# Performance work log

Hardware: AMD Instinct MI355X
Metric: run time of the kernel (lower is better)

The kernel has to match this reference:

```python
import jax, jax.numpy as jnp
import numpy as np

STRIDE = 2

def _conv_transpose3d(x, w_io, stride):
    # x: [N, I, D, H, W]; w_io: [I, O, k2, k3, k4] (torch conv_transpose layout)
    # conv_transpose == lhs-dilated conv with spatially-flipped, IO-swapped kernel
    rhs = jnp.flip(jnp.transpose(w_io, (1, 0, 2, 3, 4)), axis=(2, 3, 4))  # [O, I, k2, k3, k4]
    ks = w_io.shape[2:]
    pad = [(k - 1, k - 1) for k in ks]
    return jax.lax.conv_general_dilated(
        x, rhs, window_strides=(1, 1, 1), padding=pad,
        lhs_dilation=(stride, stride, stride),
        dimension_numbers=('NCDHW', 'OIDHW', 'NCDHW'))


def setup_inputs() -> dict:
    key = jax.random.key(0)
    k1, k2, k3 = jax.random.split(key, 3)
    B, Cin, Cout = 4, 64, 64
    K = (3, 3, 3, 3)
    L = (12, 12, 12, 12)
    init_norm = float(np.sqrt(1.0 / Cout / np.prod(K)))
    x = jax.random.normal(k1, (B, Cin, *L), dtype=jnp.float32)
    weight = init_norm * (2.0 * jax.random.normal(k2, (Cin, Cout, *K), dtype=jnp.float32) - 1.0)
    bias = init_norm * (2.0 * jax.random.normal(k3, (Cout,), dtype=jnp.float32) - 1.0)
    return {'x': x, 'weight': weight, 'bias': bias}


def reference(x, weight, bias):
    # 4D transposed convolution, stride=STRIDE, no padding/dilation, groups=1.
    B, I, L1, L2, L3, L4 = x.shape
    _, O, K1, K2, K3, K4 = weight.shape
    s = STRIDE
    o1 = (L1 - 1) * s + K1
    o2 = (L2 - 1) * s + K2
    o3 = (L3 - 1) * s + K3
    o4 = (L4 - 1) * s + K4
    # Fold first spatial dim into batch; do 3D conv_transpose over the remaining dims.
    xb = jnp.transpose(x, (0, 2, 1, 3, 4, 5)).reshape(B * L1, I, L2, L3, L4)
    out = jnp.zeros((B, O, o1, o2, o3, o4), dtype=x.dtype)
    for ik in range(K1):  # small fixed kernel loop
        y = _conv_transpose3d(xb, weight[:, :, ik], s)           # [B*L1, O, o2, o3, o4]
        y = jnp.transpose(y.reshape(B, L1, O, o2, o3, o4), (0, 2, 1, 3, 4, 5))
        out = out.at[:, :, ik:ik + L1 * s:s].add(y)              # strided scatter-add along dim 1
    out = out + bias[None, :, None, None, None, None]
    return out
```

## Files before the change

### kernel.cpp

```cpp
#include <hip/hip_runtime.h>


typedef short bf16x8 __attribute__((ext_vector_type(8)));
typedef float f32x4 __attribute__((ext_vector_type(4)));

__device__ __forceinline__ unsigned short f2bf(float f) {
    unsigned int u = __float_as_uint(f);
    u = (u + 0x7FFFu + ((u >> 16) & 1u)) >> 16;
    return (unsigned short)u;
}

__global__ __launch_bounds__(256) void wtrans_kernel(const float* __restrict__ w,
                                                     unsigned short* __restrict__ wt) {
    int tid = blockIdx.x * 256 + threadIdx.x;
    if (tid >= 81 * 64 * 64) return;
    int ci = tid & 63;
    int co = (tid >> 6) & 63;
    int kk = tid >> 12;
    wt[tid] = f2bf(w[(ci * 64 + co) * 81 + kk]);
}

__global__ __launch_bounds__(256) void xtrans_kernel(const float* __restrict__ x,
                                                     unsigned short* __restrict__ xb) {
    __shared__ unsigned short ls[144][72];
    int blk = blockIdx.x;
    int i2 = blk % 12; int t = blk / 12; int i1 = t % 12; int b = t / 12;
    int tid = threadIdx.x;
    int ci = tid >> 2, sub = tid & 3;
    const float* src = x + (size_t)b * 1327104 + (size_t)ci * 20736 + i1 * 1728 + i2 * 144 + sub * 36;
    #pragma unroll
    for (int q = 0; q < 9; ++q) {
        float4 v = *(const float4*)(src + q * 4);
        #pragma unroll
        for (int u = 0; u < 4; ++u) ls[sub * 36 + q * 4 + u][ci] = f2bf(((const float*)&v)[u]);
    }
    __syncthreads();
    unsigned short* dst = xb + (size_t)blk * 9216;
    for (int c = tid; c < 1152; c += 256) {
        int m = c >> 3, part = c & 7;
        *(bf16x8*)(dst + c * 8) = *(const bf16x8*)((const char*)ls + m * 144 + part * 16);
    }
}

#define XS_BYTES 25088
#define WS_BYTES 24576
#define SMEM_BYTES 49664

__global__ __launch_bounds__(512, 2) void convt_mfma_kernel(
        const unsigned short* __restrict__ xb,
        const unsigned short* __restrict__ wt,
        const float* __restrict__ bias,
        float* __restrict__ out) {

    __shared__ __align__(16) char smem[SMEM_BYTES];
    char* xsb = smem;
    char* wsb = smem + XS_BYTES;
    float (*stg)[625] = (float (*)[625])smem;

    int orig = blockIdx.x;
    int xcd = orig & 7, oj = orig >> 3;
    int wg = (xcd < 4 ? xcd * 313 : 1252 + (xcd - 4) * 312) + oj;
    int p2 = wg % 25; int tq = wg / 25;
    int p1 = tq % 25; int b = tq / 25;

    int i1v[2], k1v[2], n1 = 0;
    { int h = p1 >> 1, q = p1 & 1;
      for (int s = 0; s < 2 - q; ++s) { int i = h - s; if (0 <= i && i < 12) { i1v[n1] = i; k1v[n1] = 2 * s + q; ++n1; } } }
    int i2v[2], k2v[2], n2 = 0;
    { int h = p2 >> 1, q = p2 & 1;
      for (int s = 0; s < 2 - q; ++s) { int i = h - s; if (0 <= i && i < 12) { i2v[n2] = i; k2v[n2] = 2 * s + q; ++n2; } } }
    int ncomb = n1 * n2;

    int tid = threadIdx.x;
    int lane = tid & 63;
    int wave = __builtin_amdgcn_readfirstlane(tid >> 6);
    int n_lo = lane & 15, quad = lane >> 4;

    static const int NSLOT[8] = {4, 4, 5, 5, 5, 5, 6, 6};
    static const signed char SCLS[8][6] = {
        {0,0,2,2,0,0}, {0,0,2,2,0,0}, {0,0,3,3,3,0}, {0,0,3,3,3,0},
        {0,0,3,3,3,0}, {0,1,1,2,2,0}, {1,1,1,1,2,2}, {1,1,1,1,2,2}};
    static const signed char STILE[8][6] = {
        {0,1,0,1,0,0}, {2,3,2,3,0,0}, {4,5,0,1,2,0}, {6,7,3,4,5,0},
        {8,9,6,7,8,0}, {10,0,1,4,5,0}, {2,3,4,5,6,7}, {6,7,8,9,8,9}};

    int ns = NSLOT[wave];
    int use0 = 0, use1 = 0, use2 = 0, use3 = 0;
    int rbase[6]; unsigned vis = 0;
    #pragma unroll
    for (int j = 0; j < 6; ++j) {
        int c = SCLS[wave][j], t = STILE[wave][j];
        int r3 = c >> 1, r4 = c & 1;
        int n4 = 13 - r4, N = (13 - r3) * n4;
        int pos = t * 16 + n_lo;
        int cp = pos < N ? pos : N - 1;
        int pe3 = cp / n4, pe4 = cp - pe3 * n4;
        rbase[j] = (pe3 + 1) * 14 + (pe4 + 1);
        if (j < ns) {
            if (pos < N) vis |= 1u << j;
            use0 |= (c == 0); use1 |= (c == 1); use2 |= (c == 2); use3 |= (c == 3);
        }
    }

    for (int f = tid; f < XS_BYTES / 4; f += 512) ((int*)xsb)[f] = 0;

    f32x4 acc[6][4];
    #pragma unroll
    for (int mt = 0; mt < 4; ++mt) {
        #pragma unroll
        for (int rg = 0; rg < 4; ++rg) {
            float bv = bias[mt * 16 + quad * 4 + rg];
            #pragma unroll
            for (int j = 0; j < 6; ++j) acc[j][mt][rg] = bv;
        }
    }
    __syncthreads();

    for (int c = 0; c < ncomb; ++c) {
        if (c) __syncthreads();
        int c1 = c / n2, c2 = c - (c / n2) * n2;
        int i1 = i1v[c1], k1 = k1v[c1];
        int i2 = i2v[c2], k2 = k2v[c2];

        const unsigned short* xbs = xb + (size_t)((b * 12 + i1) * 12 + i2) * 9216;
        #pragma unroll
        for (int it = 0; it < 3; ++it) {
            int idx = it * 512 + tid;
            if (idx < 1152) {
                bf16x8 v = *(const bf16x8*)(xbs + idx * 8);
                int m = idx >> 3, part = idx & 7;
                int a3 = (m * 2731) >> 15, a4 = m - a3 * 12;
                int r = (a3 + 1) * 14 + a4 + 1;
                *(bf16x8*)(xsb + r * 128 + ((part ^ (r & 7)) << 4)) = v;
            }
        }

        int kb9 = (k1 * 3 + k2) * 9;
        for (int g = 0; g < 3; ++g) {
            if (g) __syncthreads();
            const unsigned short* wsrc = wt + (size_t)(kb9 + 3 * g) * 4096;
            #pragma unroll
            for (int it = 0; it < 3; ++it) {
                int idx = it * 512 + tid;
                bf16x8 v = *(const bf16x8*)(wsrc + idx * 8);
                int tap = idx >> 9, rch = idx & 511;
                int co = rch >> 3, part = rch & 7;
                *(bf16x8*)(wsb + tap * 8192 + co * 128 + ((part ^ (co & 7)) << 4)) = v;
            }
            __syncthreads();

            int p = g & 1, s3 = (g - p) >> 1;
            #pragma unroll
            for (int tap = 0; tap < 3; ++tap) {
                const int par = tap & 1;
                int any = par ? (p ? use3 : use1) : (p ? use2 : use0);
                if (!any) continue;
                int s4 = tap >> 1;
                const char* wst = wsb + tap * 8192;
                int need = 2 * p + par;
                #pragma unroll
                for (int kc = 0; kc < 2; ++kc) {
                    int pr = kc * 4 + quad;
                    int pwa = (pr ^ (n_lo & 7)) << 4;
                    bf16x8 a0  = *(const bf16x8*)(wst + n_lo * 128 + pwa);
                    bf16x8 a1  = *(const bf16x8*)(wst + n_lo * 128 + 2048 + pwa);
                    bf16x8 a2  = *(const bf16x8*)(wst + n_lo * 128 + 4096 + pwa);
                    bf16x8 a3v = *(const bf16x8*)(wst + n_lo * 128 + 6144 + pwa);
                    #pragma unroll
                    for (int j = 0; j < 6; ++j) {
                        if (j < ns && SCLS[wave][j] == need) {
                            int row = rbase[j] - s3 * 14 - s4;
                            bf16x8 bb = *(const bf16x8*)(xsb + row * 128 + ((pr ^ (row & 7)) << 4));
                            acc[j][0] = __builtin_amdgcn_mfma_f32_16x16x32_bf16(a0,  bb, acc[j][0], 0, 0, 0);
                            acc[j][1] = __builtin_amdgcn_mfma_f32_16x16x32_bf16(a1,  bb, acc[j][1], 0, 0, 0);
                            acc[j][2] = __builtin_amdgcn_mfma_f32_16x16x32_bf16(a2,  bb, acc[j][2], 0, 0, 0);
                            acc[j][3] = __builtin_amdgcn_mfma_f32_16x16x32_bf16(a3v, bb, acc[j][3], 0, 0, 0);
                        }
                    }
                }
            }
        }
    }

    __syncthreads();

    size_t obase = (size_t)b * 64 * 390625 + (size_t)(p1 * 25 + p2) * 625;
    #pragma unroll
    for (int ch = 0; ch < 4; ++ch) {
        #pragma unroll
        for (int j = 0; j < 6; ++j) {
            if ((vis >> j) & 1) {
                int cc = SCLS[wave][j];
                int r3 = cc >> 1, r4 = cc & 1;
                int rb = rbase[j] - 15;
                int pe3 = (rb * 2341) >> 15;
                int pe4 = rb - 14 * pe3;
                int p34 = (2 * pe3 + r3) * 25 + 2 * pe4 + r4;
                #pragma unroll
                for (int rg = 0; rg < 4; ++rg)
                    stg[quad * 4 + rg][p34] = acc[j][ch][rg];
            }
        }
        __syncthreads();
        for (int idx2 = tid; idx2 < 10000; idx2 += 512) {
            int co_l = idx2 / 625, e = idx2 - 625 * co_l;
            out[obase + (size_t)(ch * 16 + co_l) * 390625 + e] = stg[co_l][e];
        }
        __syncthreads();
    }
}

extern "C" void kernel_launch(void* const* d_in, const int* in_sizes, int n_in,
                              void* d_out, int out_size, void* d_ws, size_t ws_size,
                              hipStream_t stream) {
    const float* x    = (const float*)d_in[0];
    const float* w    = (const float*)d_in[1];
    const float* bias = (const float*)d_in[2];
    float* out = (float*)d_out;
    unsigned short* wt = (unsigned short*)d_ws;
    unsigned short* xbf = wt + 81 * 64 * 64;

    wtrans_kernel<<<(81 * 64 * 64 + 255) / 256, 256, 0, stream>>>(w, wt);
    xtrans_kernel<<<576, 256, 0, stream>>>(x, xbf);
    convt_mfma_kernel<<<2500, 512, 0, stream>>>(xbf, wt, bias, out);
}
```

Measured before the change: 580.9 us.

## Double-buffer weight groups with register prefetch and rebalance wave tile slots

```diff
diff --git a/kernel.cpp b/kernel.cpp
--- a/kernel.cpp
+++ b/kernel.cpp
@@ -11,13 +11,12 @@
 }
 
 __global__ __launch_bounds__(256) void wtrans_kernel(const float* __restrict__ w,
-                                                     unsigned short* __restrict__ wt) {
+                                                     unsigned short* __restrict__ wt2) {
     int tid = blockIdx.x * 256 + threadIdx.x;
     if (tid >= 81 * 64 * 64) return;
-    int ci = tid & 63;
-    int co = (tid >> 6) & 63;
-    int kk = tid >> 12;
-    wt[tid] = f2bf(w[(ci * 64 + co) * 81 + kk]);
+    int u = tid & 7, co = (tid >> 3) & 63, pr = (tid >> 9) & 7, kk = tid >> 12;
+    int ci = pr * 8 + u;
+    wt2[tid] = f2bf(w[(ci * 64 + co) * 81 + kk]);
 }
 
 __global__ __launch_bounds__(256) void xtrans_kernel(const float* __restrict__ x,
@@ -43,12 +42,12 @@
 }
 
 #define XS_BYTES 25088
-#define WS_BYTES 24576
-#define SMEM_BYTES 49664
+#define WS_HALF  24576
+#define SMEM_BYTES (XS_BYTES + 2 * WS_HALF)
 
 __global__ __launch_bounds__(512, 2) void convt_mfma_kernel(
         const unsigned short* __restrict__ xb,
-        const unsigned short* __restrict__ wt,
+        const unsigned short* __restrict__ wt2,
         const float* __restrict__ bias,
         float* __restrict__ out) {
 
@@ -76,123 +75,138 @@
     int wave = __builtin_amdgcn_readfirstlane(tid >> 6);
     int n_lo = lane & 15, quad = lane >> 4;
 
-    static const int NSLOT[8] = {4, 4, 5, 5, 5, 5, 6, 6};
-    static const signed char SCLS[8][6] = {
-        {0,0,2,2,0,0}, {0,0,2,2,0,0}, {0,0,3,3,3,0}, {0,0,3,3,3,0},
-        {0,0,3,3,3,0}, {0,1,1,2,2,0}, {1,1,1,1,2,2}, {1,1,1,1,2,2}};
-    static const signed char STILE[8][6] = {
-        {0,1,0,1,0,0}, {2,3,2,3,0,0}, {4,5,0,1,2,0}, {6,7,3,4,5,0},
-        {8,9,6,7,8,0}, {10,0,1,4,5,0}, {2,3,4,5,6,7}, {6,7,8,9,8,9}};
-
-    int ns = NSLOT[wave];
-    int use0 = 0, use1 = 0, use2 = 0, use3 = 0;
-    int rbase[6]; unsigned vis = 0;
-    #pragma unroll
-    for (int j = 0; j < 6; ++j) {
-        int c = SCLS[wave][j], t = STILE[wave][j];
-        int r3 = c >> 1, r4 = c & 1;
-        int n4 = 13 - r4, N = (13 - r3) * n4;
+    static const signed char SCLS5[8][5] = {
+        {0,0,1,2,3},{0,0,1,2,3},{0,0,1,2,3},
+        {0,1,1,2,2},{0,1,1,2,2},
+        {0,1,2,3,3},{0,1,2,3,3},{0,1,2,3,3}};
+    static const signed char STILE5[8][5] = {
+        {0,1,0,0,0},{2,3,1,1,1},{4,5,2,2,2},
+        {6,3,4,3,4},{7,5,6,5,6},
+        {8,7,7,3,4},{9,8,8,5,6},{10,9,9,7,8}};
+
+    int cmask = 0;
+    int rb128[5]; unsigned vis = 0;
+    #pragma unroll
+    for (int j = 0; j < 5; ++j) {
+        int cs = SCLS5[wave][j], t = STILE5[wave][j];
+        int r3 = cs >> 1, r4 = cs & 1;
+        int n4c = 13 - r4, Nc = (13 - r3) * n4c;
         int pos = t * 16 + n_lo;
-        int cp = pos < N ? pos : N - 1;
-        int pe3 = cp / n4, pe4 = cp - pe3 * n4;
-        rbase[j] = (pe3 + 1) * 14 + (pe4 + 1);
-        if (j < ns) {
-            if (pos < N) vis |= 1u << j;
-            use0 |= (c == 0); use1 |= (c == 1); use2 |= (c == 2); use3 |= (c == 3);
-        }
-    }
+        int cp = pos < Nc ? pos : Nc - 1;
+        int pe3 = cp / n4c, pe4 = cp - pe3 * n4c;
+        rb128[j] = ((pe3 + 1) * 14 + (pe4 + 1)) << 7;
+        if (pos < Nc) vis |= 1u << j;
+        cmask |= 1 << cs;
+    }
+
+    int xsw0, xsw1, xsw2;
+    {
+        #pragma unroll
+        for (int it = 0; it < 3; ++it) {
+            int idx = it * 512 + tid;
+            int m = idx >> 3, part = idx & 7;
+            int a3 = (m * 2731) >> 15, a4 = m - a3 * 12;
+            int r = (a3 + 1) * 14 + a4 + 1;
+            int v = r * 128 + ((part ^ (r & 7)) << 4);
+            if (it == 0) xsw0 = v; else if (it == 1) xsw1 = v; else xsw2 = v;
+        }
+    }
+    int wsw = tid * 16;
+    int abase = quad * 1024 + n_lo * 16;
 
     for (int f = tid; f < XS_BYTES / 4; f += 512) ((int*)xsb)[f] = 0;
 
-    f32x4 acc[6][4];
+    f32x4 acc[5][4];
     #pragma unroll
     for (int mt = 0; mt < 4; ++mt) {
         #pragma unroll
         for (int rg = 0; rg < 4; ++rg) {
             float bv = bias[mt * 16 + quad * 4 + rg];
             #pragma unroll
-            for (int j = 0; j < 6; ++j) acc[j][mt][rg] = bv;
+            for (int j = 0; j < 5; ++j) acc[j][mt][rg] = bv;
         }
     }
     __syncthreads();
 
+#define COMPUTE_GROUP(G, WB) do {                                              \
+    const int s3_ = (G) >> 1;                                                  \
+    _Pragma("unroll")                                                          \
+    for (int tap = 0; tap < 3; ++tap) {                                        \
+        int need = 2 * ((G) & 1) + (tap & 1), s4 = tap >> 1;                   \
+        if (!((cmask >> need) & 1)) continue;                                  \
+        const char* wt_ = (WB) + tap * 8192;                                   \
+        _Pragma("unroll")                                                      \
+        for (int kc = 0; kc < 2; ++kc) {                                       \
+            const char* ab = wt_ + kc * 4096 + abase;                          \
+            bf16x8 a0  = *(const bf16x8*)(ab);                                 \
+            bf16x8 a1  = *(const bf16x8*)(ab + 256);                           \
+            bf16x8 a2  = *(const bf16x8*)(ab + 512);                           \
+            bf16x8 a3v = *(const bf16x8*)(ab + 768);                           \
+            int prq = kc * 4 + quad;                                           \
+            _Pragma("unroll")                                                  \
+            for (int j = 0; j < 5; ++j) {                                      \
+                if (SCLS5[wave][j] == need) {                                  \
+                    int row128 = rb128[j] - ((s3_ * 14 + s4) << 7);            \
+                    int r7 = (row128 >> 7) & 7;                                \
+                    bf16x8 bb = *(const bf16x8*)(xsb + row128 + ((prq ^ r7) << 4)); \
+                    acc[j][0] = __builtin_amdgcn_mfma_f32_16x16x32_bf16(a0,  bb, acc[j][0], 0, 0, 0); \
+                    acc[j][1] = __builtin_amdgcn_mfma_f32_16x16x32_bf16(a1,  bb, acc[j][1], 0, 0, 0); \
+                    acc[j][2] = __builtin_amdgcn_mfma_f32_16x16x32_bf16(a2,  bb, acc[j][2], 0, 0, 0); \
+                    acc[j][3] = __builtin_amdgcn_mfma_f32_16x16x32_bf16(a3v, bb, acc[j][3], 0, 0, 0); \
+                }                                                              \
+            }                                                                  \
+        }                                                                      \
+    } } while (0)
+
     for (int c = 0; c < ncomb; ++c) {
-        if (c) __syncthreads();
         int c1 = c / n2, c2 = c - (c / n2) * n2;
         int i1 = i1v[c1], k1 = k1v[c1];
         int i2 = i2v[c2], k2 = k2v[c2];
-
-        const unsigned short* xbs = xb + (size_t)((b * 12 + i1) * 12 + i2) * 9216;
-        #pragma unroll
-        for (int it = 0; it < 3; ++it) {
-            int idx = it * 512 + tid;
-            if (idx < 1152) {
-                bf16x8 v = *(const bf16x8*)(xbs + idx * 8);
-                int m = idx >> 3, part = idx & 7;
-                int a3 = (m * 2731) >> 15, a4 = m - a3 * 12;
-                int r = (a3 + 1) * 14 + a4 + 1;
-                *(bf16x8*)(xsb + r * 128 + ((part ^ (r & 7)) << 4)) = v;
-            }
-        }
-
         int kb9 = (k1 * 3 + k2) * 9;
-        for (int g = 0; g < 3; ++g) {
-            if (g) __syncthreads();
-            const unsigned short* wsrc = wt + (size_t)(kb9 + 3 * g) * 4096;
-            #pragma unroll
-            for (int it = 0; it < 3; ++it) {
-                int idx = it * 512 + tid;
-                bf16x8 v = *(const bf16x8*)(wsrc + idx * 8);
-                int tap = idx >> 9, rch = idx & 511;
-                int co = rch >> 3, part = rch & 7;
-                *(bf16x8*)(wsb + tap * 8192 + co * 128 + ((part ^ (co & 7)) << 4)) = v;
-            }
-            __syncthreads();
-
-            int p = g & 1, s3 = (g - p) >> 1;
-            #pragma unroll
-            for (int tap = 0; tap < 3; ++tap) {
-                const int par = tap & 1;
-                int any = par ? (p ? use3 : use1) : (p ? use2 : use0);
-                if (!any) continue;
-                int s4 = tap >> 1;
-                const char* wst = wsb + tap * 8192;
-                int need = 2 * p + par;
-                #pragma unroll
-                for (int kc = 0; kc < 2; ++kc) {
-                    int pr = kc * 4 + quad;
-                    int pwa = (pr ^ (n_lo & 7)) << 4;
-                    bf16x8 a0  = *(const bf16x8*)(wst + n_lo * 128 + pwa);
-                    bf16x8 a1  = *(const bf16x8*)(wst + n_lo * 128 + 2048 + pwa);
-                    bf16x8 a2  = *(const bf16x8*)(wst + n_lo * 128 + 4096 + pwa);
-                    bf16x8 a3v = *(const bf16x8*)(wst + n_lo * 128 + 6144 + pwa);
-                    #pragma unroll
-                    for (int j = 0; j < 6; ++j) {
-                        if (j < ns && SCLS[wave][j] == need) {
-                            int row = rbase[j] - s3 * 14 - s4;
-                            bf16x8 bb = *(const bf16x8*)(xsb + row * 128 + ((pr ^ (row & 7)) << 4));
-                            acc[j][0] = __builtin_amdgcn_mfma_f32_16x16x32_bf16(a0,  bb, acc[j][0], 0, 0, 0);
-                            acc[j][1] = __builtin_amdgcn_mfma_f32_16x16x32_bf16(a1,  bb, acc[j][1], 0, 0, 0);
-                            acc[j][2] = __builtin_amdgcn_mfma_f32_16x16x32_bf16(a2,  bb, acc[j][2], 0, 0, 0);
-                            acc[j][3] = __builtin_amdgcn_mfma_f32_16x16x32_bf16(a3v, bb, acc[j][3], 0, 0, 0);
-                        }
-                    }
-                }
-            }
-        }
-    }
-
-    __syncthreads();
+        const bf16x8* wgsrc = (const bf16x8*)wt2 + (size_t)kb9 * 512;
+
+        bf16x8 wv0 = wgsrc[tid], wv1 = wgsrc[tid + 512], wv2 = wgsrc[tid + 1024];
+        const bf16x8* xbs = (const bf16x8*)(xb + (size_t)((b * 12 + i1) * 12 + i2) * 9216);
+        bf16x8 x0 = xbs[tid], x1 = xbs[tid + 512];
+        bf16x8 x2; if (tid < 128) x2 = xbs[tid + 1024];
+
+        char* wb0 = wsb;
+        char* wb1 = wsb + WS_HALF;
+        *(bf16x8*)(xsb + xsw0) = x0;
+        *(bf16x8*)(xsb + xsw1) = x1;
+        if (tid < 128) *(bf16x8*)(xsb + xsw2) = x2;
+        *(bf16x8*)(wb0 + wsw)         = wv0;
+        *(bf16x8*)(wb0 + wsw + 8192)  = wv1;
+        *(bf16x8*)(wb0 + wsw + 16384) = wv2;
+        wv0 = wgsrc[tid + 1536]; wv1 = wgsrc[tid + 2048]; wv2 = wgsrc[tid + 2560];
+        __syncthreads();
+
+        COMPUTE_GROUP(0, wb0);
+        *(bf16x8*)(wb1 + wsw)         = wv0;
+        *(bf16x8*)(wb1 + wsw + 8192)  = wv1;
+        *(bf16x8*)(wb1 + wsw + 16384) = wv2;
+        wv0 = wgsrc[tid + 3072]; wv1 = wgsrc[tid + 3584]; wv2 = wgsrc[tid + 4096];
+        __syncthreads();
+
+        COMPUTE_GROUP(1, wb1);
+        *(bf16x8*)(wb0 + wsw)         = wv0;
+        *(bf16x8*)(wb0 + wsw + 8192)  = wv1;
+        *(bf16x8*)(wb0 + wsw + 16384) = wv2;
+        __syncthreads();
+
+        COMPUTE_GROUP(2, wb0);
+        __syncthreads();
+    }
 
     size_t obase = (size_t)b * 64 * 390625 + (size_t)(p1 * 25 + p2) * 625;
     #pragma unroll
     for (int ch = 0; ch < 4; ++ch) {
         #pragma unroll
-        for (int j = 0; j < 6; ++j) {
+        for (int j = 0; j < 5; ++j) {
             if ((vis >> j) & 1) {
-                int cc = SCLS[wave][j];
+                int cc = SCLS5[wave][j];
                 int r3 = cc >> 1, r4 = cc & 1;
-                int rb = rbase[j] - 15;
+                int rb = (rb128[j] >> 7) - 15;
                 int pe3 = (rb * 2341) >> 15;
                 int pe4 = rb - 14 * pe3;
                 int p34 = (2 * pe3 + r3) * 25 + 2 * pe4 + r4;
@@ -217,10 +231,10 @@
     const float* w    = (const float*)d_in[1];
     const float* bias = (const float*)d_in[2];
     float* out = (float*)d_out;
-    unsigned short* wt = (unsigned short*)d_ws;
-    unsigned short* xbf = wt + 81 * 64 * 64;
-
-    wtrans_kernel<<<(81 * 64 * 64 + 255) / 256, 256, 0, stream>>>(w, wt);
+    unsigned short* wt2 = (unsigned short*)d_ws;
+    unsigned short* xbf = wt2 + 81 * 64 * 64;
+
+    wtrans_kernel<<<(81 * 64 * 64 + 255) / 256, 256, 0, stream>>>(w, wt2);
     xtrans_kernel<<<576, 256, 0, stream>>>(x, xbf);
-    convt_mfma_kernel<<<2500, 512, 0, stream>>>(xbf, wt, bias, out);
-}
+    convt_mfma_kernel<<<2500, 512, 0, stream>>>(xbf, wt2, bias, out);
+}
```

Result: no change. 569.9 us (-1.9%).
